# Kernel tuning notes

Hardware: AMD Instinct MI355X
Metric: run time of the kernel (lower is better)

## Reference

```python
import jax, jax.numpy as jnp
import numpy as np

L, D, C, H = 2, 2, 256, 128  # layers, directions, channels, hidden (= C//2, bidirectional)
B, T = 32, 1024


def setup_inputs() -> dict:
    key = jax.random.key(0)
    ks = jax.random.split(key, 5)
    k = 1.0 / np.sqrt(H)  # PyTorch LSTM init scale
    u = lambda kk, shape: jax.random.uniform(kk, shape, jnp.float32, -k, k)
    return {
        "x": jax.random.normal(ks[0], (B, C, T), jnp.float32),
        "W_ih": u(ks[1], (L, D, 4 * H, C)),  # layer1 input is concat(fwd,bwd) = C wide too
        "W_hh": u(ks[2], (L, D, 4 * H, H)),
        "b_ih": u(ks[3], (L, D, 4 * H)),
        "b_hh": u(ks[4], (L, D, 4 * H)),
    }


def _lstm_dir(xs, Wih, Whh, bih, bhh, reverse):
    # xs: [T, B, C_in] time-major; returns hidden states [T, B, H]
    Tn, Bn, _ = xs.shape
    Hh = Whh.shape[1]
    # precompute input contribution to all gates for every timestep (one big GEMM)
    gx = jnp.einsum('tbc,gc->tbg', xs, Wih) + bih + bhh  # [T, B, 4H]

    def step(carry, g):
        h, c = carry
        g = g + h @ Whh.T  # [B, 4H]
        i, f, gg, o = jnp.split(g, 4, axis=-1)  # PyTorch gate order: i, f, g, o
        c = jax.nn.sigmoid(f) * c + jax.nn.sigmoid(i) * jnp.tanh(gg)
        h = jax.nn.sigmoid(o) * jnp.tanh(c)
        return (h, c), h

    init = (jnp.zeros((Bn, Hh), xs.dtype), jnp.zeros((Bn, Hh), xs.dtype))
    _, hs = jax.lax.scan(step, init, gx, reverse=reverse)
    return hs


def reference(x, W_ih, W_hh, b_ih, b_hh):
    # x: [B, C, T] -> time-major [T, B, C] (matches x.transpose(1,2) with batch_first)
    h = jnp.transpose(x, (2, 0, 1))
    for l in range(L):
        fwd = _lstm_dir(h, W_ih[l, 0], W_hh[l, 0], b_ih[l, 0], b_hh[l, 0], False)
        bwd = _lstm_dir(h, W_ih[l, 1], W_hh[l, 1], b_ih[l, 1], b_hh[l, 1], True)
        h = jnp.concatenate([fwd, bwd], axis=-1)  # [T, B, 2H] = [T, B, C]
    # back to [B, C, T] (matches out.transpose(1,2))
    return jnp.transpose(h, (1, 2, 0))
```

## Files before the change

kernel.cpp:

```cpp
#include <hip/hip_runtime.h>
#include <cstdint>
#include <cstddef>

static constexpr int TT = 1024;
static constexpr int BB = 32;
static constexpr int CC = 256;
static constexpr int HH = 128;
static constexpr int GG = 512;
static constexpr int MM = TT * BB;

typedef float f32x4v __attribute__((ext_vector_type(4)));
typedef short bf16x8 __attribute__((ext_vector_type(8)));

__device__ __forceinline__ float fsig(float x) { return 1.f / (1.f + __expf(-x)); }
__device__ __forceinline__ float ftanh(float x) {
  float e = __expf(2.f * x);
  return 1.f - 2.f / (e + 1.f);
}
__device__ __forceinline__ ushort bf16_rn(float x) {
  union { float f; uint u; } v; v.f = x;
  const uint r = v.u + 0x7fffu + ((v.u >> 16) & 1u);
  return (ushort)(r >> 16);
}
__device__ __forceinline__ float bf16_to_f(ushort h) {
  union { uint u; float f; } v; v.u = ((uint)h) << 16;
  return v.f;
}
__device__ __forceinline__ uint pack2(ushort a, ushort b) { return (uint)a | ((uint)b << 16); }

__global__ __launch_bounds__(256) void k_transpose_cvt_in(const float* __restrict__ x,
                                                          ushort* __restrict__ xhi,
                                                          ushort* __restrict__ xlo) {
  __shared__ float tile[32][33];
  const int t0 = blockIdx.x * 32, c0 = blockIdx.y * 32, b = blockIdx.z;
  const int tx = threadIdx.x, ty = threadIdx.y;
#pragma unroll
  for (int i = 0; i < 4; i++) {
    const int cc = ty + i * 8;
    tile[cc][tx] = x[((size_t)b * CC + (c0 + cc)) * TT + t0 + tx];
  }
  __syncthreads();
#pragma unroll
  for (int i = 0; i < 4; i++) {
    const int tt = ty + i * 8;
    const float v = tile[tx][tt];
    const ushort hi = bf16_rn(v);
    const size_t idx = ((size_t)(t0 + tt) * BB + b) * CC + c0 + tx;
    xhi[idx] = hi;
    xlo[idx] = bf16_rn(v - bf16_to_f(hi));
  }
}

__global__ __launch_bounds__(256) void k_transpose_out(const float* __restrict__ h2,
                                                       float* __restrict__ out) {
  __shared__ float tile[32][33];
  const int t0 = blockIdx.x * 32, c0 = blockIdx.y * 32, b = blockIdx.z;
  const int tx = threadIdx.x, ty = threadIdx.y;
#pragma unroll
  for (int i = 0; i < 4; i++) {
    const int tt = ty + i * 8;
    tile[tt][tx] = h2[((size_t)(t0 + tt) * BB + b) * CC + c0 + tx];
  }
  __syncthreads();
#pragma unroll
  for (int i = 0; i < 4; i++) {
    const int cc = ty + i * 8;
    out[((size_t)b * CC + (c0 + cc)) * TT + t0 + tx] = tile[tx][cc];
  }
}

__global__ __launch_bounds__(256) void k_gemm_mfma(const ushort* __restrict__ Ahi,
                                                   const ushort* __restrict__ Alo,
                                                   const float* __restrict__ W,
                                                   const float* __restrict__ bih,
                                                   const float* __restrict__ bhh,
                                                   float* __restrict__ gx) {
  const int d = blockIdx.z;
  const int g0 = blockIdx.x * 64;
  const int m0 = blockIdx.y * 128;
  const float* Wd = W + (size_t)d * GG * CC;

  __shared__ ushort Ah[128][64];
  __shared__ ushort Al[128][64];
  __shared__ ushort Bh[64][64];
  __shared__ ushort Bl[64][64];

  const int tid = threadIdx.x;
  const int lane = tid & 63;
  const int wid = tid >> 6;
  const int wm = (wid >> 1) * 64;
  const int wg = (wid & 1) * 32;

  f32x4v acc[4][2] = {};

  for (int k0 = 0; k0 < CC; k0 += 64) {
    __syncthreads();
#pragma unroll
    for (int c = 0; c < 4; c++) {
      const int f8 = c * 256 + tid;
      const int r = f8 >> 3;
      const int kb = f8 & 7;
      const int sw = (kb ^ (r & 7)) << 3;
      const uint4 vh = *(const uint4*)&Ahi[(size_t)(m0 + r) * CC + k0 + kb * 8];
      const uint4 vl = *(const uint4*)&Alo[(size_t)(m0 + r) * CC + k0 + kb * 8];
      *(uint4*)&Ah[r][sw] = vh;
      *(uint4*)&Al[r][sw] = vl;
    }
#pragma unroll
    for (int c = 0; c < 4; c++) {
      const int f4 = c * 256 + tid;
      const int g = f4 >> 4;
      const int k4 = f4 & 15;
      const float4 wv = *(const float4*)&Wd[(size_t)(g0 + g) * CC + k0 + k4 * 4];
      ushort h0 = bf16_rn(wv.x), h1 = bf16_rn(wv.y), h2 = bf16_rn(wv.z), h3 = bf16_rn(wv.w);
      ushort l0 = bf16_rn(wv.x - bf16_to_f(h0)), l1 = bf16_rn(wv.y - bf16_to_f(h1));
      ushort l2 = bf16_rn(wv.z - bf16_to_f(h2)), l3 = bf16_rn(wv.w - bf16_to_f(h3));
      const int off = (((k4 >> 1) ^ (g & 7)) << 3) | ((k4 & 1) * 4);
      uint2 ph; ph.x = pack2(h0, h1); ph.y = pack2(h2, h3);
      uint2 pl; pl.x = pack2(l0, l1); pl.y = pack2(l2, l3);
      *(uint2*)&Bh[g][off] = ph;
      *(uint2*)&Bl[g][off] = pl;
    }
    __syncthreads();
#pragma unroll
    for (int h = 0; h < 2; h++) {
      const int kb = h * 4 + (lane >> 4);
      bf16x8 afh[4], afl[4], bfh[2], bfl[2];
#pragma unroll
      for (int i = 0; i < 4; i++) {
        const int row = wm + i * 16 + (lane & 15);
        const int sw = (kb ^ (row & 7)) << 3;
        afh[i] = *(const bf16x8*)&Ah[row][sw];
        afl[i] = *(const bf16x8*)&Al[row][sw];
      }
#pragma unroll
      for (int j = 0; j < 2; j++) {
        const int gr = wg + j * 16 + (lane & 15);
        const int sw = (kb ^ (gr & 7)) << 3;
        bfh[j] = *(const bf16x8*)&Bh[gr][sw];
        bfl[j] = *(const bf16x8*)&Bl[gr][sw];
      }
#pragma unroll
      for (int i = 0; i < 4; i++)
#pragma unroll
        for (int j = 0; j < 2; j++) {
          acc[i][j] = __builtin_amdgcn_mfma_f32_16x16x32_bf16(afh[i], bfh[j], acc[i][j], 0, 0, 0);
          acc[i][j] = __builtin_amdgcn_mfma_f32_16x16x32_bf16(afh[i], bfl[j], acc[i][j], 0, 0, 0);
          acc[i][j] = __builtin_amdgcn_mfma_f32_16x16x32_bf16(afl[i], bfh[j], acc[i][j], 0, 0, 0);
        }
    }
  }
  const int col = lane & 15;
  const int rbase = (lane >> 4) * 4;
#pragma unroll
  for (int j = 0; j < 2; j++) {
    const int g = g0 + wg + j * 16 + col;
    const float bias = bih[d * GG + g] + bhh[d * GG + g];
#pragma unroll
    for (int i = 0; i < 4; i++) {
      const int mrow = m0 + wm + i * 16 + rbase;
#pragma unroll
      for (int rr = 0; rr < 4; rr++)
        gx[((size_t)d * MM + mrow + rr) * GG + g] = acc[i][j][rr] + bias;
    }
  }
}

__global__ __launch_bounds__(512, 1) void k_lstm_rec(const float* __restrict__ gx,
                                                     const float* __restrict__ Whh,
                                                     float* __restrict__ hf32,
                                                     ushort* __restrict__ hhi,
                                                     ushort* __restrict__ hlo,
                                                     int store_bf16) {
  const int b = blockIdx.x & 31;
  const int d = blockIdx.x >> 5;
  const int tid = threadIdx.x;
  const int q = tid >> 7;
  const int j = tid & 127;
  __shared__ __align__(16) float h_s[HH];
  __shared__ __align__(16) float part[4][HH][4];

  float4 w4[4][8];
  {
    const float* base = Whh + (size_t)d * GG * HH;
#pragma unroll
    for (int gi = 0; gi < 4; gi++) {
      const float4* wrow = (const float4*)(base + (size_t)(gi * HH + j) * HH + q * 32);
#pragma unroll
      for (int k = 0; k < 8; k++) w4[gi][k] = wrow[k];
    }
  }
#pragma unroll
  for (int gi = 0; gi < 4; gi++)
#pragma unroll
    for (int k = 0; k < 8; k++)
      asm volatile("" : "+v"(w4[gi][k].x), "+v"(w4[gi][k].y), "+v"(w4[gi][k].z), "+v"(w4[gi][k].w));

  if (tid < HH) h_s[tid] = 0.f;
  float c = 0.f;

  const float* gxb = gx + ((size_t)d * TT * BB + b) * (size_t)GG;
  const size_t stride = (size_t)BB * GG;
  int t = d ? (TT - 1) : 0;
  const int tdir = d ? -1 : 1;
  const bool is_act = (tid < HH);

  float gxc0 = 0.f, gxc1 = 0.f, gxc2 = 0.f, gxc3 = 0.f;
  if (is_act) {
    const float* g0 = gxb + (size_t)t * stride + j;
    gxc0 = g0[0]; gxc1 = g0[HH]; gxc2 = g0[2 * HH]; gxc3 = g0[3 * HH];
  }
  __syncthreads();

  for (int s = 0; s < TT; s++) {
    float gxn0 = 0.f, gxn1 = 0.f, gxn2 = 0.f, gxn3 = 0.f;
    if (is_act && s + 1 < TT) {
      const float* g0 = gxb + (size_t)(t + tdir) * stride + j;
      gxn0 = g0[0]; gxn1 = g0[HH]; gxn2 = g0[2 * HH]; gxn3 = g0[3 * HH];
    }

    const float4* hq = (const float4*)(h_s + q * 32);
    float a0 = 0.f, a1 = 0.f, a2 = 0.f, a3 = 0.f;
#pragma unroll
    for (int k = 0; k < 8; k++) {
      const float4 hv = hq[k];
      a0 = fmaf(w4[0][k].x, hv.x, a0); a0 = fmaf(w4[0][k].y, hv.y, a0);
      a0 = fmaf(w4[0][k].z, hv.z, a0); a0 = fmaf(w4[0][k].w, hv.w, a0);
      a1 = fmaf(w4[1][k].x, hv.x, a1); a1 = fmaf(w4[1][k].y, hv.y, a1);
      a1 = fmaf(w4[1][k].z, hv.z, a1); a1 = fmaf(w4[1][k].w, hv.w, a1);
      a2 = fmaf(w4[2][k].x, hv.x, a2); a2 = fmaf(w4[2][k].y, hv.y, a2);
      a2 = fmaf(w4[2][k].z, hv.z, a2); a2 = fmaf(w4[2][k].w, hv.w, a2);
      a3 = fmaf(w4[3][k].x, hv.x, a3); a3 = fmaf(w4[3][k].y, hv.y, a3);
      a3 = fmaf(w4[3][k].z, hv.z, a3); a3 = fmaf(w4[3][k].w, hv.w, a3);
    }
    *(float4*)&part[q][j][0] = make_float4(a0, a1, a2, a3);
    __syncthreads();

    if (is_act) {
      const float4 p0 = *(const float4*)&part[0][j][0];
      const float4 p1 = *(const float4*)&part[1][j][0];
      const float4 p2 = *(const float4*)&part[2][j][0];
      const float4 p3 = *(const float4*)&part[3][j][0];
      const float i_g = fsig(p0.x + p1.x + p2.x + p3.x + gxc0);
      const float f_g = fsig(p0.y + p1.y + p2.y + p3.y + gxc1);
      const float g_g = ftanh(p0.z + p1.z + p2.z + p3.z + gxc2);
      const float o_g = fsig(p0.w + p1.w + p2.w + p3.w + gxc3);
      c = f_g * c + i_g * g_g;
      const float h = o_g * ftanh(c);
      h_s[j] = h;
      const size_t idx = ((size_t)t * BB + b) * CC + d * HH + j;
      if (store_bf16) {
        const ushort hi = bf16_rn(h);
        hhi[idx] = hi;
        hlo[idx] = bf16_rn(h - bf16_to_f(hi));
      } else {
        hf32[idx] = h;
      }
    }
    __syncthreads();
    gxc0 = gxn0; gxc1 = gxn1; gxc2 = gxn2; gxc3 = gxn3;
    t += tdir;
  }
}

extern "C" void kernel_launch(void* const* d_in, const int* in_sizes, int n_in,
                              void* d_out, int out_size, void* d_ws, size_t ws_size,
                              hipStream_t stream) {
  const float* x    = (const float*)d_in[0];
  const float* W_ih = (const float*)d_in[1];
  const float* W_hh = (const float*)d_in[2];
  const float* b_ih = (const float*)d_in[3];
  const float* b_hh = (const float*)d_in[4];
  float* out = (float*)d_out;

  if (ws_size < (size_t)160 * 1024 * 1024) return;

  char* ws = (char*)d_ws;
  ushort* abf_hi = (ushort*)ws;
  ushort* abf_lo = (ushort*)(ws + (size_t)16 * 1024 * 1024);
  float*  h2     = (float*)ws;
  float*  gxbuf  = (float*)(ws + (size_t)32 * 1024 * 1024);

  const dim3 tb(32, 8);
  const dim3 tg(TT / 32, CC / 32, BB);
  const dim3 gemm_grid(GG / 64, MM / 128, 2);

  k_transpose_cvt_in<<<tg, tb, 0, stream>>>(x, abf_hi, abf_lo);
  k_gemm_mfma<<<gemm_grid, 256, 0, stream>>>(abf_hi, abf_lo, W_ih, b_ih, b_hh, gxbuf);
  k_lstm_rec<<<64, 512, 0, stream>>>(gxbuf, W_hh, nullptr, abf_hi, abf_lo, 1);
  k_gemm_mfma<<<gemm_grid, 256, 0, stream>>>(abf_hi, abf_lo, W_ih + 2 * GG * CC,
                                             b_ih + 2 * GG, b_hh + 2 * GG, gxbuf);
  k_lstm_rec<<<64, 512, 0, stream>>>(gxbuf, W_hh + 2 * GG * HH, h2, nullptr, nullptr, 0);
  k_transpose_out<<<tg, tb, 0, stream>>>(h2, out);
}
```

Baseline: 1.799 ms.

## Interleave two batch elements per LSTM recurrence block to overlap matvec and gates

The recurrence kernel now gives each block two batch elements and alternates between them. The hidden-state dot product for one element is computed in the same barrier interval as the gate activations of the other. The aim is to hide the serial dot-then-activation latency chain through instruction-level overlap. In exchange, half as many blocks are launched, so each block runs twice as many dependent half-steps, which could lengthen the critical path if the overlap is poor.

Measured after the change: 3.247 ms. +80.5%, slower.

```diff
diff --git a/kernel.cpp b/kernel.cpp
--- a/kernel.cpp
+++ b/kernel.cpp
@@ -166,19 +166,40 @@
   }
 }
 
-__global__ __launch_bounds__(512, 1) void k_lstm_rec(const float* __restrict__ gx,
-                                                     const float* __restrict__ Whh,
-                                                     float* __restrict__ hf32,
-                                                     ushort* __restrict__ hhi,
-                                                     ushort* __restrict__ hlo,
-                                                     int store_bf16) {
-  const int b = blockIdx.x & 31;
-  const int d = blockIdx.x >> 5;
+__device__ __forceinline__ void rec_dot4(const float* __restrict__ hsrc,
+                                         float* __restrict__ pdst,
+                                         const float4 (&w4)[4][8]) {
+  const float4* hq = (const float4*)hsrc;
+  float a0 = 0.f, a1 = 0.f, a2 = 0.f, a3 = 0.f;
+#pragma unroll
+  for (int k = 0; k < 8; k++) {
+    const float4 hv = hq[k];
+    a0 = fmaf(w4[0][k].x, hv.x, a0); a0 = fmaf(w4[0][k].y, hv.y, a0);
+    a0 = fmaf(w4[0][k].z, hv.z, a0); a0 = fmaf(w4[0][k].w, hv.w, a0);
+    a1 = fmaf(w4[1][k].x, hv.x, a1); a1 = fmaf(w4[1][k].y, hv.y, a1);
+    a1 = fmaf(w4[1][k].z, hv.z, a1); a1 = fmaf(w4[1][k].w, hv.w, a1);
+    a2 = fmaf(w4[2][k].x, hv.x, a2); a2 = fmaf(w4[2][k].y, hv.y, a2);
+    a2 = fmaf(w4[2][k].z, hv.z, a2); a2 = fmaf(w4[2][k].w, hv.w, a2);
+    a3 = fmaf(w4[3][k].x, hv.x, a3); a3 = fmaf(w4[3][k].y, hv.y, a3);
+    a3 = fmaf(w4[3][k].z, hv.z, a3); a3 = fmaf(w4[3][k].w, hv.w, a3);
+  }
+  *(float4*)pdst = make_float4(a0, a1, a2, a3);
+}
+
+__global__ __launch_bounds__(512, 1) void k_lstm_rec_pair(const float* __restrict__ gx,
+                                                          const float* __restrict__ Whh,
+                                                          float* __restrict__ hf32,
+                                                          ushort* __restrict__ hhi,
+                                                          ushort* __restrict__ hlo,
+                                                          int store_bf16) {
+  const int pair = blockIdx.x & 15;
+  const int d = blockIdx.x >> 4;
+  const int b0 = pair * 2, b1 = pair * 2 + 1;
   const int tid = threadIdx.x;
   const int q = tid >> 7;
   const int j = tid & 127;
-  __shared__ __align__(16) float h_s[HH];
-  __shared__ __align__(16) float part[4][HH][4];
+  __shared__ __align__(16) float h_s[2][HH];
+  __shared__ __align__(16) float part[2][4][HH][4];
 
   float4 w4[4][8];
   {
@@ -196,59 +217,49 @@
     for (int k = 0; k < 8; k++)
       asm volatile("" : "+v"(w4[gi][k].x), "+v"(w4[gi][k].y), "+v"(w4[gi][k].z), "+v"(w4[gi][k].w));
 
-  if (tid < HH) h_s[tid] = 0.f;
-  float c = 0.f;
-
-  const float* gxb = gx + ((size_t)d * TT * BB + b) * (size_t)GG;
+  if (tid < HH) { h_s[0][tid] = 0.f; h_s[1][tid] = 0.f; }
+  float cA = 0.f, cB = 0.f;
+
+  const float* gxA = gx + ((size_t)d * TT * BB + b0) * (size_t)GG;
+  const float* gxB = gx + ((size_t)d * TT * BB + b1) * (size_t)GG;
   const size_t stride = (size_t)BB * GG;
   int t = d ? (TT - 1) : 0;
   const int tdir = d ? -1 : 1;
   const bool is_act = (tid < HH);
 
-  float gxc0 = 0.f, gxc1 = 0.f, gxc2 = 0.f, gxc3 = 0.f;
+  float gA0 = 0.f, gA1 = 0.f, gA2 = 0.f, gA3 = 0.f;
+  float gB0 = 0.f, gB1 = 0.f, gB2 = 0.f, gB3 = 0.f;
   if (is_act) {
-    const float* g0 = gxb + (size_t)t * stride + j;
-    gxc0 = g0[0]; gxc1 = g0[HH]; gxc2 = g0[2 * HH]; gxc3 = g0[3 * HH];
+    const float* a = gxA + (size_t)t * stride + j;
+    gA0 = a[0]; gA1 = a[HH]; gA2 = a[2 * HH]; gA3 = a[3 * HH];
+    const float* bq = gxB + (size_t)t * stride + j;
+    gB0 = bq[0]; gB1 = bq[HH]; gB2 = bq[2 * HH]; gB3 = bq[3 * HH];
   }
   __syncthreads();
 
+  rec_dot4(&h_s[0][q * 32], &part[0][q][j][0], w4);
+  __syncthreads();
+
   for (int s = 0; s < TT; s++) {
-    float gxn0 = 0.f, gxn1 = 0.f, gxn2 = 0.f, gxn3 = 0.f;
-    if (is_act && s + 1 < TT) {
-      const float* g0 = gxb + (size_t)(t + tdir) * stride + j;
-      gxn0 = g0[0]; gxn1 = g0[HH]; gxn2 = g0[2 * HH]; gxn3 = g0[3 * HH];
-    }
-
-    const float4* hq = (const float4*)(h_s + q * 32);
-    float a0 = 0.f, a1 = 0.f, a2 = 0.f, a3 = 0.f;
-#pragma unroll
-    for (int k = 0; k < 8; k++) {
-      const float4 hv = hq[k];
-      a0 = fmaf(w4[0][k].x, hv.x, a0); a0 = fmaf(w4[0][k].y, hv.y, a0);
-      a0 = fmaf(w4[0][k].z, hv.z, a0); a0 = fmaf(w4[0][k].w, hv.w, a0);
-      a1 = fmaf(w4[1][k].x, hv.x, a1); a1 = fmaf(w4[1][k].y, hv.y, a1);
-      a1 = fmaf(w4[1][k].z, hv.z, a1); a1 = fmaf(w4[1][k].w, hv.w, a1);
-      a2 = fmaf(w4[2][k].x, hv.x, a2); a2 = fmaf(w4[2][k].y, hv.y, a2);
-      a2 = fmaf(w4[2][k].z, hv.z, a2); a2 = fmaf(w4[2][k].w, hv.w, a2);
-      a3 = fmaf(w4[3][k].x, hv.x, a3); a3 = fmaf(w4[3][k].y, hv.y, a3);
-      a3 = fmaf(w4[3][k].z, hv.z, a3); a3 = fmaf(w4[3][k].w, hv.w, a3);
-    }
-    *(float4*)&part[q][j][0] = make_float4(a0, a1, a2, a3);
-    __syncthreads();
-
+    float gAn0 = 0.f, gAn1 = 0.f, gAn2 = 0.f, gAn3 = 0.f;
+    rec_dot4(&h_s[1][q * 32], &part[1][q][j][0], w4);
     if (is_act) {
-      const float4 p0 = *(const float4*)&part[0][j][0];
-      const float4 p1 = *(const float4*)&part[1][j][0];
-      const float4 p2 = *(const float4*)&part[2][j][0];
-      const float4 p3 = *(const float4*)&part[3][j][0];
-      const float i_g = fsig(p0.x + p1.x + p2.x + p3.x + gxc0);
-      const float f_g = fsig(p0.y + p1.y + p2.y + p3.y + gxc1);
-      const float g_g = ftanh(p0.z + p1.z + p2.z + p3.z + gxc2);
-      const float o_g = fsig(p0.w + p1.w + p2.w + p3.w + gxc3);
-      c = f_g * c + i_g * g_g;
-      const float h = o_g * ftanh(c);
-      h_s[j] = h;
-      const size_t idx = ((size_t)t * BB + b) * CC + d * HH + j;
+      if (s + 1 < TT) {
+        const float* a = gxA + (size_t)(t + tdir) * stride + j;
+        gAn0 = a[0]; gAn1 = a[HH]; gAn2 = a[2 * HH]; gAn3 = a[3 * HH];
+      }
+      const float4 p0 = *(const float4*)&part[0][0][j][0];
+      const float4 p1 = *(const float4*)&part[0][1][j][0];
+      const float4 p2 = *(const float4*)&part[0][2][j][0];
+      const float4 p3 = *(const float4*)&part[0][3][j][0];
+      const float i_g = fsig(p0.x + p1.x + p2.x + p3.x + gA0);
+      const float f_g = fsig(p0.y + p1.y + p2.y + p3.y + gA1);
+      const float g_g = ftanh(p0.z + p1.z + p2.z + p3.z + gA2);
+      const float o_g = fsig(p0.w + p1.w + p2.w + p3.w + gA3);
+      cA = f_g * cA + i_g * g_g;
+      const float h = o_g * ftanh(cA);
+      h_s[0][j] = h;
+      const size_t idx = ((size_t)t * BB + b0) * CC + d * HH + j;
       if (store_bf16) {
         const ushort hi = bf16_rn(h);
         hhi[idx] = hi;
@@ -258,7 +269,38 @@
       }
     }
     __syncthreads();
-    gxc0 = gxn0; gxc1 = gxn1; gxc2 = gxn2; gxc3 = gxn3;
+
+    float gBn0 = 0.f, gBn1 = 0.f, gBn2 = 0.f, gBn3 = 0.f;
+    if (s + 1 < TT) rec_dot4(&h_s[0][q * 32], &part[0][q][j][0], w4);
+    if (is_act) {
+      if (s + 1 < TT) {
+        const float* bq = gxB + (size_t)(t + tdir) * stride + j;
+        gBn0 = bq[0]; gBn1 = bq[HH]; gBn2 = bq[2 * HH]; gBn3 = bq[3 * HH];
+      }
+      const float4 p0 = *(const float4*)&part[1][0][j][0];
+      const float4 p1 = *(const float4*)&part[1][1][j][0];
+      const float4 p2 = *(const float4*)&part[1][2][j][0];
+      const float4 p3 = *(const float4*)&part[1][3][j][0];
+      const float i_g = fsig(p0.x + p1.x + p2.x + p3.x + gB0);
+      const float f_g = fsig(p0.y + p1.y + p2.y + p3.y + gB1);
+      const float g_g = ftanh(p0.z + p1.z + p2.z + p3.z + gB2);
+      const float o_g = fsig(p0.w + p1.w + p2.w + p3.w + gB3);
+      cB = f_g * cB + i_g * g_g;
+      const float h = o_g * ftanh(cB);
+      h_s[1][j] = h;
+      const size_t idx = ((size_t)t * BB + b1) * CC + d * HH + j;
+      if (store_bf16) {
+        const ushort hi = bf16_rn(h);
+        hhi[idx] = hi;
+        hlo[idx] = bf16_rn(h - bf16_to_f(hi));
+      } else {
+        hf32[idx] = h;
+      }
+    }
+    __syncthreads();
+
+    gA0 = gAn0; gA1 = gAn1; gA2 = gAn2; gA3 = gAn3;
+    gB0 = gBn0; gB1 = gBn1; gB2 = gBn2; gB3 = gBn3;
     t += tdir;
   }
 }
@@ -287,9 +329,9 @@
 
   k_transpose_cvt_in<<<tg, tb, 0, stream>>>(x, abf_hi, abf_lo);
   k_gemm_mfma<<<gemm_grid, 256, 0, stream>>>(abf_hi, abf_lo, W_ih, b_ih, b_hh, gxbuf);
-  k_lstm_rec<<<64, 512, 0, stream>>>(gxbuf, W_hh, nullptr, abf_hi, abf_lo, 1);
+  k_lstm_rec_pair<<<32, 512, 0, stream>>>(gxbuf, W_hh, nullptr, abf_hi, abf_lo, 1);
   k_gemm_mfma<<<gemm_grid, 256, 0, stream>>>(abf_hi, abf_lo, W_ih + 2 * GG * CC,
                                              b_ih + 2 * GG, b_hh + 2 * GG, gxbuf);
-  k_lstm_rec<<<64, 512, 0, stream>>>(gxbuf, W_hh + 2 * GG * HH, h2, nullptr, nullptr, 0);
+  k_lstm_rec_pair<<<32, 512, 0, stream>>>(gxbuf, W_hh + 2 * GG * HH, h2, nullptr, nullptr, 0);
   k_transpose_out<<<tg, tb, 0, stream>>>(h2, out);
 }
```
